# Kernel optimization log

Measured on AMD Instinct MI355X. Metric: run time of the kernel, lower is better.

Reference implementation:

```python
import jax, jax.numpy as jnp
from jax import lax
import numpy as np

EPS = 1e-5
BETA = 0.2

def _bn(x, g, b):
    # training-mode BatchNorm2d: batch stats over (N,H,W), biased variance
    m = jnp.mean(x, (0, 2, 3), keepdims=True)
    v = jnp.mean((x - m) ** 2, (0, 2, 3), keepdims=True)
    return (x - m) / jnp.sqrt(v + EPS) * g[None, :, None, None] + b[None, :, None, None]

def _conv(x, w, b, stride, pad):
    y = lax.conv_general_dilated(x, w, (stride, stride), ((pad, pad), (pad, pad)),
                                 dimension_numbers=('NCHW', 'OIHW', 'NCHW'))
    return y + b[None, :, None, None]

def _convT(x, w, b):
    # ConvTranspose2d(k=4, s=2, p=1): flip kernel, swap in/out, lhs_dilation=2, pad k-1-p=2
    wf = jnp.flip(w, (2, 3)).transpose(1, 0, 2, 3)  # torch [in,out,kh,kw] -> OIHW
    y = lax.conv_general_dilated(x, wf, (1, 1), ((2, 2), (2, 2)), lhs_dilation=(2, 2),
                                 dimension_numbers=('NCHW', 'OIHW', 'NCHW'))
    return y + b[None, :, None, None]

def setup_inputs() -> dict:
    key = jax.random.key(0)
    ks = jax.random.split(key, 16)
    s = 0.05
    d = {
        'x':     jax.random.normal(ks[0], (64, 1, 256, 256), jnp.float32),
        'w1':    jax.random.normal(ks[1], (16, 1, 4, 4)) * s, 'b1': jnp.zeros((16,)),
        'g1':    jnp.ones((16,)), 'be1': jnp.zeros((16,)),
        'w2':    jax.random.normal(ks[2], (4, 16, 4, 4)) * s, 'b2': jnp.zeros((4,)),
        'g2':    jnp.ones((4,)), 'be2': jnp.zeros((4,)),
        'wpre':  jax.random.normal(ks[3], (2, 4, 1, 1)) * s, 'bpre': jnp.zeros((2,)),
        'emb':   jax.random.normal(ks[4], (64, 2)) * s,
        'wpost': jax.random.normal(ks[5], (4, 2, 1, 1)) * s, 'bpost': jnp.zeros((4,)),
        'wd1':   jax.random.normal(ks[6], (4, 16, 4, 4)) * s, 'bd1': jnp.zeros((16,)),
        'g3':    jnp.ones((16,)), 'be3': jnp.zeros((16,)),
        'wd2':   jax.random.normal(ks[7], (16, 1, 4, 4)) * s, 'bd2': jnp.zeros((1,)),
    }
    return d

def reference(x, w1, b1, g1, be1, w2, b2, g2, be2, wpre, bpre, emb,
              wpost, bpost, wd1, bd1, g3, be3, wd2, bd2):
    h = jax.nn.relu(_bn(_conv(x, w1, b1, 2, 1), g1, be1))
    h = jax.nn.relu(_bn(_conv(h, w2, b2, 2, 1), g2, be2))
    z = _conv(h, wpre, bpre, 1, 0)                 # [B,2,H/4,W/4]
    B, C, H, W = z.shape
    zf = z.transpose(0, 2, 3, 1).reshape(B, H * W, C)  # [B,HW,C]
    # squared euclidean distances (argmin equal to argmin of cdist)
    d2 = (jnp.sum(zf * zf, -1, keepdims=True)
          - 2.0 * jnp.einsum('bnc,kc->bnk', zf, emb)
          + jnp.sum(emb * emb, -1))                # [B,HW,K]
    idx = jnp.argmin(d2, axis=-1)                  # [B,HW]
    q = emb[idx]                                   # gather [B,HW,C]
    commitment_loss = jnp.mean((lax.stop_gradient(q) - zf) ** 2)
    codebook_loss = jnp.mean((q - lax.stop_gradient(zf)) ** 2)
    q_st = zf + lax.stop_gradient(q - zf)          # straight-through
    qo = q_st.reshape(B, H, W, C).transpose(0, 3, 1, 2)
    di = _conv(qo, wpost, bpost, 1, 0)
    h2 = jax.nn.relu(_bn(_convT(di, wd1, bd1), g3, be3))
    out = jnp.tanh(_convT(h2, wd2, bd2))           # [B,1,256,256]
    recon_loss = jnp.mean((x - out) ** 2)
    quantize_loss = codebook_loss + BETA * commitment_loss + recon_loss
    return out, quantize_loss
```

## Files before the change

### kernel.cpp

```cpp
#include <hip/hip_runtime.h>
#include <hip/hip_bf16.h>

typedef const float* fp32p;


__device__ __forceinline__ float4 f4fma(float s, float4 w, float4 a){
  a.x = fmaf(s,w.x,a.x); a.y = fmaf(s,w.y,a.y);
  a.z = fmaf(s,w.z,a.z); a.w = fmaf(s,w.w,a.w);
  return a;
}

__device__ __forceinline__ float dot4acc(float4 d, float4 w, float a){
  a = fmaf(d.x,w.x,a); a = fmaf(d.y,w.y,a);
  a = fmaf(d.z,w.z,a); a = fmaf(d.w,w.w,a);
  return a;
}

__device__ __forceinline__ double block_sum_all_d(double v, double* sm){
  #pragma unroll
  for (int m=1;m<64;m<<=1) v += __shfl_xor(v, m, 64);
  int lane = threadIdx.x & 63, wid = threadIdx.x >> 6;
  if (lane==0) sm[wid] = v;
  __syncthreads();
  return sm[0]+sm[1]+sm[2]+sm[3];
}

__global__ __launch_bounds__(256) void k_conv1v2(fp32p x, fp32p w1, fp32p b1,
                                                 float* __restrict__ h1, float* __restrict__ part){
  __shared__ float sx[34][67];
  __shared__ float sw[16][16];
  __shared__ float sb[16];
  __shared__ float red[4][32];
  int tid = threadIdx.x;
  { int co = tid & 15, tap = tid >> 4;
    sw[tap][co] = w1[co*16 + tap];
    if (tid < 16) sb[tid] = b1[tid]; }
  int b = blockIdx.x;
  int n = b>>5, t = b&31, ty = t>>2, tx = t&3;
  int OY = ty*16, OX = tx*32;
  int gy0 = OY*2-1, gx0 = OX*2-1;
  const float* xb = x + n*65536;
  for (int p=tid; p<2244; p+=256){
    int r = p/66, c = p - r*66;
    int gy = gy0+r, gx = gx0+c;
    sx[r][c] = ((unsigned)gy < 256u && (unsigned)gx < 256u) ? xb[gy*256+gx] : 0.f;
  }
  __syncthreads();
  int oyl = tid>>4, oxl = tid&15;
  float4 a00 = *(float4*)&sb[0], a01 = *(float4*)&sb[4],
         a02 = *(float4*)&sb[8], a03 = *(float4*)&sb[12];
  float4 a10 = a00, a11 = a01, a12 = a02, a13 = a03;
  #pragma unroll
  for (int ky=0; ky<4; ky++){
    const float* sxr = &sx[oyl*2+ky][4*oxl];
    #pragma unroll
    for (int kx=0; kx<4; kx++){
      const float4* wr = (const float4*)&sw[ky*4+kx][0];
      float4 w0 = wr[0], w1v = wr[1], w2 = wr[2], w3 = wr[3];
      float v0 = sxr[kx];
      a00 = f4fma(v0, w0, a00); a01 = f4fma(v0, w1v, a01);
      a02 = f4fma(v0, w2, a02); a03 = f4fma(v0, w3, a03);
      float v1 = sxr[2+kx];
      a10 = f4fma(v1, w0, a10); a11 = f4fma(v1, w1v, a11);
      a12 = f4fma(v1, w2, a12); a13 = f4fma(v1, w3, a13);
    }
  }
  int gid = (n*128+OY+oyl)*128 + OX + 2*oxl;
  float4* o = (float4*)&h1[(unsigned)gid*16u];
  o[0]=a00; o[1]=a01; o[2]=a02; o[3]=a03;
  o[4]=a10; o[5]=a11; o[6]=a12; o[7]=a13;
  float f0[16], f1[16];
  *(float4*)&f0[0]=a00; *(float4*)&f0[4]=a01; *(float4*)&f0[8]=a02; *(float4*)&f0[12]=a03;
  *(float4*)&f1[0]=a10; *(float4*)&f1[4]=a11; *(float4*)&f1[8]=a12; *(float4*)&f1[12]=a13;
  int lane = tid & 63, wid = tid >> 6;
  #pragma unroll
  for (int c=0;c<16;c++){
    float s = f0[c] + f1[c];
    float q = fmaf(f0[c],f0[c], f1[c]*f1[c]);
    #pragma unroll
    for (int m=1;m<64;m<<=1){ s += __shfl_xor(s,m,64); q += __shfl_xor(q,m,64); }
    if (lane==0){ red[wid][c]=s; red[wid][16+c]=q; }
  }
  __syncthreads();
  if (tid<32){
    float v = red[0][tid]+red[1][tid]+red[2][tid]+red[3][tid];
    part[tid*2048 + blockIdx.x] = v;
  }
}

__global__ __launch_bounds__(256) void k_redf(const float* __restrict__ part, int N, int nch,
    fp32p g, fp32p be, double cnt, float* __restrict__ sc, float* __restrict__ sh){
  __shared__ double sm[4];
  int c = blockIdx.x;
  double s=0.0, q=0.0;
  for (int i=threadIdx.x;i<N;i+=256){ s += (double)part[c*N+i]; q += (double)part[(nch+c)*N+i]; }
  s = block_sum_all_d(s, sm); __syncthreads();
  q = block_sum_all_d(q, sm);
  if (threadIdx.x==0){
    double m = s/cnt;
    double var = q/cnt - m*m;
    double sd = (double)g[c] / sqrt(var + 1e-5);
    sc[c] = (float)sd;
    sh[c] = (float)((double)be[c] - m*sd);
  }
}

__global__ __launch_bounds__(256) void k_redd(const float* __restrict__ part, int N, int nch,
    fp32p g, fp32p be, double cnt, double* __restrict__ sc, double* __restrict__ sh){
  __shared__ double sm[4];
  int c = blockIdx.x;
  double s=0.0, q=0.0;
  for (int i=threadIdx.x;i<N;i+=256){ s += (double)part[c*N+i]; q += (double)part[(nch+c)*N+i]; }
  s = block_sum_all_d(s, sm); __syncthreads();
  q = block_sum_all_d(q, sm);
  if (threadIdx.x==0){
    double m = s/cnt;
    double var = q/cnt - m*m;
    double sd = (double)g[c] / sqrt(var + 1e-5);
    sc[c] = sd;
    sh[c] = (double)be[c] - m*sd;
  }
}

__global__ __launch_bounds__(256) void k_conv2(const float* __restrict__ h1, fp32p w2, fp32p b2,
    const float* __restrict__ sc1, const float* __restrict__ sh1,
    float* __restrict__ h2, float* __restrict__ part){
  __shared__ float sw[16][16][4];
  __shared__ float sb[4];
  __shared__ float red[4][8];
  int tid = threadIdx.x;
  for (int j=tid;j<1024;j+=256){
    int co=j&3, ci=(j>>2)&15, tap=j>>6;
    sw[tap][ci][co] = w2[(co*16+ci)*16 + tap];
  }
  if (tid<4) sb[tid]=b2[tid];
  __syncthreads();
  float sc[16], sh[16];
  #pragma unroll
  for (int c=0;c<16;c++){ sc[c]=sc1[c]; sh[c]=sh1[c]; }
  int gid = blockIdx.x*256+tid;
  int ox = gid&63, oy=(gid>>6)&63, n=gid>>12;
  float4 acc = *(float4*)&sb[0];
  #pragma unroll
  for (int ky=0;ky<4;ky++){
    int iy = oy*2-1+ky;
    if ((unsigned)iy >= 128u) continue;
    #pragma unroll
    for (int kx=0;kx<4;kx++){
      int ix = ox*2-1+kx;
      if ((unsigned)ix >= 128u) continue;
      const float4* hp = (const float4*)&h1[((n*128+iy)*128+ix)*16];
      const float4* wt = (const float4*)&sw[ky*4+kx][0][0];
      #pragma unroll
      for (int c4=0;c4<4;c4++){
        float4 hv = hp[c4];
        float v;
        v = fmaxf(fmaf(hv.x, sc[c4*4+0], sh[c4*4+0]), 0.f); acc = f4fma(v, wt[c4*4+0], acc);
        v = fmaxf(fmaf(hv.y, sc[c4*4+1], sh[c4*4+1]), 0.f); acc = f4fma(v, wt[c4*4+1], acc);
        v = fmaxf(fmaf(hv.z, sc[c4*4+2], sh[c4*4+2]), 0.f); acc = f4fma(v, wt[c4*4+2], acc);
        v = fmaxf(fmaf(hv.w, sc[c4*4+3], sh[c4*4+3]), 0.f); acc = f4fma(v, wt[c4*4+3], acc);
      }
    }
  }
  *(float4*)&h2[(unsigned)gid*4u] = acc;
  float aa[4]; *(float4*)&aa[0] = acc;
  int lane = tid & 63, wid = tid >> 6;
  #pragma unroll
  for (int c=0;c<4;c++){
    float s = aa[c], q = aa[c]*aa[c];
    #pragma unroll
    for (int m=1;m<64;m<<=1){ s += __shfl_xor(s,m,64); q += __shfl_xor(q,m,64); }
    if (lane==0){ red[wid][c]=s; red[wid][4+c]=q; }
  }
  __syncthreads();
  if (tid<8){
    float v = red[0][tid]+red[1][tid]+red[2][tid]+red[3][tid];
    part[tid*1024 + blockIdx.x] = v;
  }
}

__global__ __launch_bounds__(256) void k_vq(const float* __restrict__ h2,
    const double* __restrict__ bnd,
    fp32p wpre, fp32p bpre, fp32p emb, fp32p wpost, fp32p bpost,
    float* __restrict__ di, double* __restrict__ redE){
  __shared__ double se[128];
  __shared__ double sm[4];
  int tid = threadIdx.x;
  if (tid < 128) se[tid] = (double)emb[tid];
  __syncthreads();
  double sc[4], sh[4];
  #pragma unroll
  for (int c=0;c<4;c++){ sc[c]=bnd[c]; sh[c]=bnd[4+c]; }
  double wa0=wpre[0], wa1=wpre[1], wa2=wpre[2], wa3=wpre[3];
  double wb0=wpre[4], wb1=wpre[5], wb2=wpre[6], wb3=wpre[7];
  double bp0=bpre[0], bp1=bpre[1];
  double p00=wpost[0], p01=wpost[1];
  double p10=wpost[2], p11=wpost[3];
  double p20=wpost[4], p21=wpost[5];
  double p30=wpost[6], p31=wpost[7];
  double bq0=bpost[0], bq1=bpost[1], bq2=bpost[2], bq3=bpost[3];
  int p = blockIdx.x*256 + tid;
  float4 hv = *(const float4*)&h2[(unsigned)p*4u];
  double h0 = fmax(fma((double)hv.x, sc[0], sh[0]), 0.0);
  double h1v = fmax(fma((double)hv.y, sc[1], sh[1]), 0.0);
  double h2v = fmax(fma((double)hv.z, sc[2], sh[2]), 0.0);
  double h3v = fmax(fma((double)hv.w, sc[3], sh[3]), 0.0);
  double z0 = bp0 + wa0*h0 + wa1*h1v + wa2*h2v + wa3*h3v;
  double z1 = bp1 + wb0*h0 + wb1*h1v + wb2*h2v + wb3*h3v;
  double best = 1e300; int bi = 0;
  #pragma unroll
  for (int k=0;k<64;k++){
    double d0 = z0 - se[2*k], d1 = z1 - se[2*k+1];
    double d = fma(d0,d0, d1*d1);
    if (d < best){ best = d; bi = k; }
  }
  double qv0 = se[2*bi], qv1 = se[2*bi+1];
  double e0 = qv0-z0, e1 = qv1-z1;
  double lsum = fma(e0,e0, e1*e1);
  float4 o;
  o.x = (float)(fma(p00,qv0, fma(p01,qv1, bq0)));
  o.y = (float)(fma(p10,qv0, fma(p11,qv1, bq1)));
  o.z = (float)(fma(p20,qv0, fma(p21,qv1, bq2)));
  o.w = (float)(fma(p30,qv0, fma(p31,qv1, bq3)));
  *(float4*)&di[(unsigned)p*4u] = o;
  double tot = block_sum_all_d(lsum, sm);
  if (tid==0) redE[blockIdx.x] = tot;
}

__global__ __launch_bounds__(256) void k_stats3v2(const float* __restrict__ di, fp32p wd1, fp32p bd1,
                                                  float* __restrict__ part){
  __shared__ float sw[16][4][16];
  __shared__ float sb[16];
  __shared__ float red[4][32];
  int tid = threadIdx.x;
  for (int j=tid; j<1024; j+=256){
    int co = j & 15, ci = (j>>4)&3, tap = j>>6;
    sw[tap][ci][co] = wd1[(ci*16+co)*16 + tap];
  }
  if (tid<16) sb[tid] = bd1[tid];
  __syncthreads();
  int gid = blockIdx.x*256 + tid;
  int k  = gid & 63;
  int oy = (gid >> 6) & 127;
  int n  = gid >> 13;
  float4 e0 = *(float4*)&sb[0], e1 = *(float4*)&sb[4],
         e2 = *(float4*)&sb[8], e3 = *(float4*)&sb[12];
  float4 o0 = e0, o1 = e1, o2 = e2, o3 = e3;
  int py = (oy+1)&1;
  #pragma unroll
  for (int jt=0;jt<2;jt++){
    int ky = py + 2*jt;
    int iy = (oy+1-ky) >> 1;
    if ((unsigned)iy >= 64u) continue;
    const float4* drow = (const float4*)&di[((n*64+iy)*64)*4];
    float4 dm = (k>=1) ? drow[k-1] : make_float4(0.f,0.f,0.f,0.f);
    float4 d0 = drow[k];
    float4 dp = (k<63) ? drow[k+1] : make_float4(0.f,0.f,0.f,0.f);
    {
      int tap = ky*4 + 1;
      float vv[4] = {d0.x, d0.y, d0.z, d0.w};
      #pragma unroll
      for (int ci=0;ci<4;ci++){
        const float4* wr = (const float4*)&sw[tap][ci][0];
        e0 = f4fma(vv[ci], wr[0], e0); e1 = f4fma(vv[ci], wr[1], e1);
        e2 = f4fma(vv[ci], wr[2], e2); e3 = f4fma(vv[ci], wr[3], e3);
      }
      tap = ky*4 + 3;
      float vm[4] = {dm.x, dm.y, dm.z, dm.w};
      #pragma unroll
      for (int ci=0;ci<4;ci++){
        const float4* wr = (const float4*)&sw[tap][ci][0];
        e0 = f4fma(vm[ci], wr[0], e0); e1 = f4fma(vm[ci], wr[1], e1);
        e2 = f4fma(vm[ci], wr[2], e2); e3 = f4fma(vm[ci], wr[3], e3);
      }
    }
    {
      int tap = ky*4 + 0;
      float vp[4] = {dp.x, dp.y, dp.z, dp.w};
      #pragma unroll
      for (int ci=0;ci<4;ci++){
        const float4* wr = (const float4*)&sw[tap][ci][0];
        o0 = f4fma(vp[ci], wr[0], o0); o1 = f4fma(vp[ci], wr[1], o1);
        o2 = f4fma(vp[ci], wr[2], o2); o3 = f4fma(vp[ci], wr[3], o3);
      }
      tap = ky*4 + 2;
      float v0[4] = {d0.x, d0.y, d0.z, d0.w};
      #pragma unroll
      for (int ci=0;ci<4;ci++){
        const float4* wr = (const float4*)&sw[tap][ci][0];
        o0 = f4fma(v0[ci], wr[0], o0); o1 = f4fma(v0[ci], wr[1], o1);
        o2 = f4fma(v0[ci], wr[2], o2); o3 = f4fma(v0[ci], wr[3], o3);
      }
    }
  }
  float fe[16], fo[16];
  *(float4*)&fe[0]=e0; *(float4*)&fe[4]=e1; *(float4*)&fe[8]=e2; *(float4*)&fe[12]=e3;
  *(float4*)&fo[0]=o0; *(float4*)&fo[4]=o1; *(float4*)&fo[8]=o2; *(float4*)&fo[12]=o3;
  int lane = tid & 63, wid = tid >> 6;
  #pragma unroll
  for (int c=0;c<16;c++){
    float s = fe[c] + fo[c];
    float q = fmaf(fe[c],fe[c], fo[c]*fo[c]);
    #pragma unroll
    for (int m=1;m<64;m<<=1){ s += __shfl_xor(s,m,64); q += __shfl_xor(q,m,64); }
    if (lane==0){ red[wid][c]=s; red[wid][16+c]=q; }
  }
  __syncthreads();
  if (tid<32){
    float v = red[0][tid]+red[1][tid]+red[2][tid]+red[3][tid];
    part[tid*2048 + blockIdx.x] = v;
  }
}

__global__ __launch_bounds__(256) void k_fuseT8(const float* __restrict__ di,
    fp32p wd1, fp32p bd1, fp32p wd2, fp32p bd2,
    const float* __restrict__ sc3, const float* __restrict__ sh3,
    fp32p x, float* __restrict__ out, double* __restrict__ redH){
  __shared__ float swt[1024];
  __shared__ float sb1[16];
  __shared__ float sw2[256];
  __shared__ float h3q[4][18][19][4];
  __shared__ double smd[4];
  int tid = threadIdx.x;
  for (int j=tid; j<1024; j+=256){
    int co = j & 15, ci = (j>>4)&3, kx = (j>>6)&3, ky = j>>8;
    swt[j] = wd1[((ci*16+co)*4+ky)*4+kx];
  }
  { int ci = tid & 15, kx = (tid>>4)&3, ky = tid>>6;
    sw2[tid] = wd2[ci*16 + ky*4 + kx]; }
  if (tid<16) sb1[tid] = bd1[tid];
  float s3[16], h3s[16];
  #pragma unroll
  for (int c=0;c<16;c++){ s3[c]=sc3[c]; h3s[c]=sh3[c]; }
  int b = blockIdx.x;
  int n = b>>6, ty=(b>>3)&7, tx=b&7;
  int OY=ty*32, OX=tx*32;
  int R0=ty*16-1, C0=tx*16-1;
  __syncthreads();
  int clsA = tid >> 6;
  int prA = clsA >> 1, pcA = clsA & 1;
  for (int it2=0; it2<2; it2++){
    int idx = (tid & 63) + it2*64;
    if (idx < 81){
      int u = idx/9, v = idx - u*9;
      int rr = 2*u + prA, cc = 2*v + pcA;
      int r = R0 + rr, c = C0 + cc;
      float vo[16];
      if ((unsigned)r < 128u && (unsigned)c < 128u){
        float acc[16];
        #pragma unroll
        for (int ch=0;ch<16;ch++) acc[ch]=sb1[ch];
        #pragma unroll
        for (int j=0;j<2;j++){
          int iy = ty*8 + u - j;
          if ((unsigned)iy >= 64u) continue;
          #pragma unroll
          for (int i=0;i<2;i++){
            int ix = tx*8 + v - i;
            if ((unsigned)ix >= 64u) continue;
            float4 dv = *(const float4*)&di[((n*64+iy)*64+ix)*4];
            const float* wb = &swt[(((prA+2*j)*4+(pcA+2*i))*4)*16];
            float vv[4] = {dv.x, dv.y, dv.z, dv.w};
            #pragma unroll
            for (int ci=0;ci<4;ci++){
              #pragma unroll
              for (int co=0;co<16;co++)
                acc[co] = fmaf(vv[ci], wb[ci*16+co], acc[co]);
            }
          }
        }
        #pragma unroll
        for (int ch=0;ch<16;ch++) vo[ch] = fmaxf(fmaf(acc[ch], s3[ch], h3s[ch]), 0.f);
      } else {
        #pragma unroll
        for (int ch=0;ch<16;ch++) vo[ch]=0.f;
      }
      #pragma unroll
      for (int q=0;q<4;q++)
        *(float4*)&h3q[q][rr][cc][0] = make_float4(vo[4*q],vo[4*q+1],vo[4*q+2],vo[4*q+3]);
    }
  }
  __syncthreads();
  int lane = tid & 63, wv = tid >> 6;
  int ri = lane >> 3, tc = lane & 7;
  int row = (wv>>1)*16 + ri*2 + (wv&1);
  int oy = OY + row, ox0 = OX + tc*4;
  int py = (oy+1)&1;
  int rr0 = ((oy + 1 - py) >> 1) - R0;
  int c0 = tc*2;
  float bias = bd2[0];
  float a0=bias, a1=bias, a2=bias, a3=bias;
  #pragma unroll
  for (int q=0;q<4;q++){
    #pragma unroll
    for (int j=0;j<2;j++){
      int rr = rr0 - j;
      int kyb = (py + 2*j)*4;
      float4 d0 = *(float4*)&h3q[q][rr][c0+0][0];
      float4 d1 = *(float4*)&h3q[q][rr][c0+1][0];
      float4 d2 = *(float4*)&h3q[q][rr][c0+2][0];
      float4 d3 = *(float4*)&h3q[q][rr][c0+3][0];
      {
        float4 wA = *(float4*)&sw2[(kyb+1)*16 + q*4];
        float4 wB = *(float4*)&sw2[(kyb+3)*16 + q*4];
        a0 = dot4acc(d1, wA, a0); a0 = dot4acc(d0, wB, a0);
        a2 = dot4acc(d2, wA, a2); a2 = dot4acc(d1, wB, a2);
      }
      {
        float4 wA = *(float4*)&sw2[(kyb+0)*16 + q*4];
        float4 wB = *(float4*)&sw2[(kyb+2)*16 + q*4];
        a1 = dot4acc(d2, wA, a1); a1 = dot4acc(d1, wB, a1);
        a3 = dot4acc(d3, wA, a3); a3 = dot4acc(d2, wB, a3);
      }
    }
  }
  int base = (n*256+oy)*256 + ox0;
  float4 xv = *(const float4*)&x[base];
  float av[4] = {a0,a1,a2,a3};
  float r4[4];
  double rsum = 0.0;
  #pragma unroll
  for (int k=0;k<4;k++){
    float e = __expf(2.f*av[k]);
    float t = 1.f - 2.f/(e+1.f);
    r4[k] = t;
    float xd = (k==0?xv.x:k==1?xv.y:k==2?xv.z:xv.w);
    double dd = (double)xd - (double)t;
    rsum = fma(dd,dd,rsum);
  }
  *(float4*)&out[base] = make_float4(r4[0],r4[1],r4[2],r4[3]);
  double tot = block_sum_all_d(rsum, smd);
  if (tid==0) redH[b] = tot;
}

__global__ __launch_bounds__(256) void k_final(const double* __restrict__ redE, const double* __restrict__ redH,
                                               float* __restrict__ out, int out_size){
  __shared__ double sm[4];
  int tid = threadIdx.x;
  double a = 0.0;
  for (int i=tid;i<1024;i+=256) a += redE[i];
  double b = 0.0;
  for (int i=tid;i<4096;i+=256) b += redH[i];
  double ta = block_sum_all_d(a, sm);
  __syncthreads();
  double tb = block_sum_all_d(b, sm);
  if (tid==0){
    double loss = 1.2*ta/524288.0 + tb/4194304.0;
    out[out_size-1] = (float)loss;
  }
}

extern "C" void kernel_launch(void* const* d_in, const int* in_sizes, int n_in,
                              void* d_out, int out_size, void* d_ws, size_t ws_size,
                              hipStream_t stream) {
  (void)ws_size;
  int I[20];
  for (int i=0;i<20;i++) I[i]=i;
  if (n_in >= 20 && in_sizes[0] != 4194304 && in_sizes[19] == 4194304){
    static const int remap[20] = {19,13,0,10,4,14,1,11,5,18,8,9,17,7,15,2,12,6,16,3};
    for (int i=0;i<20;i++) I[i]=remap[i];
  }
  fp32p x    = (fp32p)d_in[I[0]];
  fp32p w1   = (fp32p)d_in[I[1]],  b1 = (fp32p)d_in[I[2]],  g1 = (fp32p)d_in[I[3]],  be1 = (fp32p)d_in[I[4]];
  fp32p w2   = (fp32p)d_in[I[5]],  b2 = (fp32p)d_in[I[6]],  g2 = (fp32p)d_in[I[7]],  be2 = (fp32p)d_in[I[8]];
  fp32p wpre = (fp32p)d_in[I[9]],  bpre = (fp32p)d_in[I[10]], emb = (fp32p)d_in[I[11]];
  fp32p wpost= (fp32p)d_in[I[12]], bpost= (fp32p)d_in[I[13]];
  fp32p wd1  = (fp32p)d_in[I[14]], bd1 = (fp32p)d_in[I[15]], g3 = (fp32p)d_in[I[16]], be3 = (fp32p)d_in[I[17]];
  fp32p wd2  = (fp32p)d_in[I[18]], bd2 = (fp32p)d_in[I[19]];

  char* wsb = (char*)d_ws;
  float* h1    = (float*)(wsb);
  float* h2    = (float*)(wsb + 67108864);
  float* di    = (float*)(wsb + 71303168);
  float* bnf   = (float*)(wsb + 75497472);
  double* bnd  = (double*)(wsb + 75497728);
  double* redE = (double*)(wsb + 75497792);
  double* redH = (double*)(wsb + 67108864);
  float* part1 = (float*)(wsb + 67108864);
  float* part2 = (float*)(wsb + 71303168);
  float* part3 = (float*)(wsb);
  float* sc1 = bnf, *sh1 = bnf+16, *sc3 = bnf+32, *sh3 = bnf+48;
  float* out = (float*)d_out;

  k_conv1v2 <<<2048,256,0,stream>>>(x, w1, b1, h1, part1);
  k_redf    <<<16,256,0,stream>>>(part1, 2048, 16, g1, be1, 1048576.0, sc1, sh1);
  k_conv2   <<<1024,256,0,stream>>>(h1, w2, b2, sc1, sh1, h2, part2);
  k_redd    <<<4,256,0,stream>>>(part2, 1024, 4, g2, be2, 262144.0, bnd, bnd+4);
  k_vq      <<<1024,256,0,stream>>>(h2, bnd, wpre, bpre, emb, wpost, bpost, di, redE);
  k_stats3v2<<<2048,256,0,stream>>>(di, wd1, bd1, part3);
  k_redf    <<<16,256,0,stream>>>(part3, 2048, 16, g3, be3, 1048576.0, sc3, sh3);
  k_fuseT8  <<<4096,256,0,stream>>>(di, wd1, bd1, wd2, bd2, sc3, sh3, x, out, redH);
  k_final   <<<1,256,0,stream>>>(redE, redH, out, out_size);
}
```

Before: 184.4 us.

## Compute two adjacent conv2 outputs per thread to reuse overlapping input columns

Each thread in the second strided conv now produces two horizontally adjacent output pixels, so the overlapping input columns (6 loaded instead of 8 per row) are read and BN+ReLU-transformed once and shared between both accumulators. The grid is halved to 512 blocks and the partial-sum stride in the BN reduction is updated to match. This cuts global loads and the per-element normalize work, at the cost of more registers per thread and fewer threads in flight.

Result: slower. 477.8 us (+159.1%).

```diff
diff --git a/kernel.cpp b/kernel.cpp
--- a/kernel.cpp
+++ b/kernel.cpp
@@ -122,7 +122,7 @@
   }
 }
 
-__global__ __launch_bounds__(256) void k_conv2(const float* __restrict__ h1, fp32p w2, fp32p b2,
+__global__ __launch_bounds__(256) void k_conv2v2(const float* __restrict__ h1, fp32p w2, fp32p b2,
     const float* __restrict__ sc1, const float* __restrict__ sh1,
     float* __restrict__ h2, float* __restrict__ part){
   __shared__ float sw[16][16][4];
@@ -139,35 +139,69 @@
   #pragma unroll
   for (int c=0;c<16;c++){ sc[c]=sc1[c]; sh[c]=sh1[c]; }
   int gid = blockIdx.x*256+tid;
-  int ox = gid&63, oy=(gid>>6)&63, n=gid>>12;
-  float4 acc = *(float4*)&sb[0];
-  #pragma unroll
-  for (int ky=0;ky<4;ky++){
+  int k = gid & 31, oy = (gid>>5)&63, n = gid>>11;
+  float4 ae = *(float4*)&sb[0];
+  float4 ao = ae;
+
+  #define LR(DST, COL, ROK, ROWP) { \
+    bool ok_ = (ROK) && ((unsigned)(COL) < 128u); \
+    const float4* hp_ = (const float4*)&(ROWP)[(ok_?(COL):0)*16]; \
+    float4 t0_=hp_[0], t1_=hp_[1], t2_=hp_[2], t3_=hp_[3]; \
+    DST[0].x = ok_ ? fmaxf(fmaf(t0_.x, sc[0],  sh[0]),  0.f) : 0.f; \
+    DST[0].y = ok_ ? fmaxf(fmaf(t0_.y, sc[1],  sh[1]),  0.f) : 0.f; \
+    DST[0].z = ok_ ? fmaxf(fmaf(t0_.z, sc[2],  sh[2]),  0.f) : 0.f; \
+    DST[0].w = ok_ ? fmaxf(fmaf(t0_.w, sc[3],  sh[3]),  0.f) : 0.f; \
+    DST[1].x = ok_ ? fmaxf(fmaf(t1_.x, sc[4],  sh[4]),  0.f) : 0.f; \
+    DST[1].y = ok_ ? fmaxf(fmaf(t1_.y, sc[5],  sh[5]),  0.f) : 0.f; \
+    DST[1].z = ok_ ? fmaxf(fmaf(t1_.z, sc[6],  sh[6]),  0.f) : 0.f; \
+    DST[1].w = ok_ ? fmaxf(fmaf(t1_.w, sc[7],  sh[7]),  0.f) : 0.f; \
+    DST[2].x = ok_ ? fmaxf(fmaf(t2_.x, sc[8],  sh[8]),  0.f) : 0.f; \
+    DST[2].y = ok_ ? fmaxf(fmaf(t2_.y, sc[9],  sh[9]),  0.f) : 0.f; \
+    DST[2].z = ok_ ? fmaxf(fmaf(t2_.z, sc[10], sh[10]), 0.f) : 0.f; \
+    DST[2].w = ok_ ? fmaxf(fmaf(t2_.w, sc[11], sh[11]), 0.f) : 0.f; \
+    DST[3].x = ok_ ? fmaxf(fmaf(t3_.x, sc[12], sh[12]), 0.f) : 0.f; \
+    DST[3].y = ok_ ? fmaxf(fmaf(t3_.y, sc[13], sh[13]), 0.f) : 0.f; \
+    DST[3].z = ok_ ? fmaxf(fmaf(t3_.z, sc[14], sh[14]), 0.f) : 0.f; \
+    DST[3].w = ok_ ? fmaxf(fmaf(t3_.w, sc[15], sh[15]), 0.f) : 0.f; }
+
+  #define TAP(ACC, D, TP) { const float4* wt_ = (const float4*)&sw[TP][0][0]; \
+    ACC = f4fma(D[0].x, wt_[0],  ACC); ACC = f4fma(D[0].y, wt_[1],  ACC); \
+    ACC = f4fma(D[0].z, wt_[2],  ACC); ACC = f4fma(D[0].w, wt_[3],  ACC); \
+    ACC = f4fma(D[1].x, wt_[4],  ACC); ACC = f4fma(D[1].y, wt_[5],  ACC); \
+    ACC = f4fma(D[1].z, wt_[6],  ACC); ACC = f4fma(D[1].w, wt_[7],  ACC); \
+    ACC = f4fma(D[2].x, wt_[8],  ACC); ACC = f4fma(D[2].y, wt_[9],  ACC); \
+    ACC = f4fma(D[2].z, wt_[10], ACC); ACC = f4fma(D[2].w, wt_[11], ACC); \
+    ACC = f4fma(D[3].x, wt_[12], ACC); ACC = f4fma(D[3].y, wt_[13], ACC); \
+    ACC = f4fma(D[3].z, wt_[14], ACC); ACC = f4fma(D[3].w, wt_[15], ACC); }
+
+  #pragma unroll
+  for (int ky=0; ky<4; ky++){
     int iy = oy*2-1+ky;
-    if ((unsigned)iy >= 128u) continue;
-    #pragma unroll
-    for (int kx=0;kx<4;kx++){
-      int ix = ox*2-1+kx;
-      if ((unsigned)ix >= 128u) continue;
-      const float4* hp = (const float4*)&h1[((n*128+iy)*128+ix)*16];
-      const float4* wt = (const float4*)&sw[ky*4+kx][0][0];
-      #pragma unroll
-      for (int c4=0;c4<4;c4++){
-        float4 hv = hp[c4];
-        float v;
-        v = fmaxf(fmaf(hv.x, sc[c4*4+0], sh[c4*4+0]), 0.f); acc = f4fma(v, wt[c4*4+0], acc);
-        v = fmaxf(fmaf(hv.y, sc[c4*4+1], sh[c4*4+1]), 0.f); acc = f4fma(v, wt[c4*4+1], acc);
-        v = fmaxf(fmaf(hv.z, sc[c4*4+2], sh[c4*4+2]), 0.f); acc = f4fma(v, wt[c4*4+2], acc);
-        v = fmaxf(fmaf(hv.w, sc[c4*4+3], sh[c4*4+3]), 0.f); acc = f4fma(v, wt[c4*4+3], acc);
-      }
-    }
-  }
-  *(float4*)&h2[(unsigned)gid*4u] = acc;
-  float aa[4]; *(float4*)&aa[0] = acc;
+    bool rok = (unsigned)iy < 128u;
+    int iyc = rok ? iy : 0;
+    const float* rowp = &h1[((n*128+iyc)*128)*16];
+    float4 A[4], B[4], C[4], D[4], E[4], F[4];
+    LR(A, 4*k-1, rok, rowp); LR(C, 4*k+1, rok, rowp);
+    TAP(ae, A, ky*4+0);      TAP(ao, C, ky*4+0);
+    LR(B, 4*k,   rok, rowp); LR(D, 4*k+2, rok, rowp);
+    TAP(ae, B, ky*4+1);      TAP(ao, D, ky*4+1);
+    LR(E, 4*k+3, rok, rowp);
+    TAP(ae, C, ky*4+2);      TAP(ao, E, ky*4+2);
+    LR(F, 4*k+4, rok, rowp);
+    TAP(ae, D, ky*4+3);      TAP(ao, F, ky*4+3);
+  }
+  #undef LR
+  #undef TAP
+  unsigned obase = ((unsigned)((n*64+oy)*64) + 2u*k)*4u;
+  *(float4*)&h2[obase]   = ae;
+  *(float4*)&h2[obase+4] = ao;
+  float fe[4], fo[4];
+  *(float4*)&fe[0] = ae; *(float4*)&fo[0] = ao;
   int lane = tid & 63, wid = tid >> 6;
   #pragma unroll
   for (int c=0;c<4;c++){
-    float s = aa[c], q = aa[c]*aa[c];
+    float s = fe[c] + fo[c];
+    float q = fmaf(fe[c],fe[c], fo[c]*fo[c]);
     #pragma unroll
     for (int m=1;m<64;m<<=1){ s += __shfl_xor(s,m,64); q += __shfl_xor(q,m,64); }
     if (lane==0){ red[wid][c]=s; red[wid][4+c]=q; }
@@ -175,7 +209,7 @@
   __syncthreads();
   if (tid<8){
     float v = red[0][tid]+red[1][tid]+red[2][tid]+red[3][tid];
-    part[tid*1024 + blockIdx.x] = v;
+    part[tid*512 + blockIdx.x] = v;
   }
 }
 
@@ -484,8 +518,8 @@
 
   k_conv1v2 <<<2048,256,0,stream>>>(x, w1, b1, h1, part1);
   k_redf    <<<16,256,0,stream>>>(part1, 2048, 16, g1, be1, 1048576.0, sc1, sh1);
-  k_conv2   <<<1024,256,0,stream>>>(h1, w2, b2, sc1, sh1, h2, part2);
-  k_redd    <<<4,256,0,stream>>>(part2, 1024, 4, g2, be2, 262144.0, bnd, bnd+4);
+  k_conv2v2 <<<512,256,0,stream>>>(h1, w2, b2, sc1, sh1, h2, part2);
+  k_redd    <<<4,256,0,stream>>>(part2, 512, 4, g2, be2, 262144.0, bnd, bnd+4);
   k_vq      <<<1024,256,0,stream>>>(h2, bnd, wpre, bpre, emb, wpost, bpost, di, redE);
   k_stats3v2<<<2048,256,0,stream>>>(di, wd1, bd1, part3);
   k_redf    <<<16,256,0,stream>>>(part3, 2048, 16, g3, be3, 1048576.0, sc3, sh3);
```
